# Optimization experiments

Measured on AMD Instinct MI355X. Metric: run time of the kernel, lower is better.

## Reference

```python
import jax, jax.numpy as jnp
import numpy as np

B, N, P, H, E, M, O, T = 4, 128, 512, 64, 32, 64, 64, 64

def _normalize(v, axis=-1, eps=1e-12):
    n = jnp.sqrt(jnp.sum(v * v, axis=axis, keepdims=True))
    return v / jnp.maximum(n, eps)

def _quat_mul(a, b):
    aw, ax, ay, az = a[..., 0], a[..., 1], a[..., 2], a[..., 3]
    bw, bx, by, bz = b[..., 0], b[..., 1], b[..., 2], b[..., 3]
    return jnp.stack([
        aw*bw - ax*bx - ay*by - az*bz,
        aw*bx + ax*bw + ay*bz - az*by,
        aw*by - ax*bz + ay*bw + az*bx,
        aw*bz + ax*by - ay*bx + az*bw], axis=-1)

def _quat_conj(q):
    return q * jnp.array([1.0, -1.0, -1.0, -1.0], dtype=q.dtype)

def _quat_rotate(q, v):
    # rotate vectors v [...,3] by unit quaternions q [...,4] in (w,x,y,z)
    qv = q[..., 1:]
    w = q[..., :1]
    t = 2.0 * jnp.cross(qv, v)
    return v + w * t + jnp.cross(qv, t)

def _mlp(x, W1, b1, W2, b2):
    return jax.nn.relu(x @ W1 + b1) @ W2 + b2

def setup_inputs():
    key = jax.random.key(0)
    ks = jax.random.split(key, 20)
    def w(k, i, o):
        return (jax.random.normal(k, (i, o), jnp.float32) / np.sqrt(i)).astype(jnp.float32)
    inp = dict(
        q=_normalize(jax.random.normal(ks[0], (B, N, 4), jnp.float32)),
        x=jax.random.normal(ks[1], (B, N, 3), jnp.float32),
        torsions=jax.random.normal(ks[2], (B, N, 7, 2), jnp.float32),
        h=jax.random.normal(ks[3], (B, N, H), jnp.float32),
        e=jax.random.normal(ks[4], (B, N, N, E), jnp.float32),
        node_mask=jnp.ones((B, N), bool),
        pocket_q=_normalize(jax.random.normal(ks[5], (B, P, 4), jnp.float32)),
        pocket_x=jax.random.normal(ks[6], (B, P, 3), jnp.float32),
        pocket_e=jax.random.normal(ks[7], (B, N, P, E), jnp.float32),
        pocket_h=jax.random.normal(ks[8], (B, P, H), jnp.float32),
        pocket_mask=jnp.ones((B, P), bool),
        Wm1=w(ks[9], 2 * H + E + 9, T), bm1=jnp.zeros((T,), jnp.float32),
        Wm2=w(ks[10], T, M), bm2=jnp.zeros((M,), jnp.float32),
        Wf1=w(ks[11], H + M, T), bf1=jnp.zeros((T,), jnp.float32),
        Wf2=w(ks[12], T, O), bf2=jnp.zeros((O,), jnp.float32),
        Wx1=w(ks[13], M, T), bx1=jnp.zeros((T,), jnp.float32),
        Wx2=w(ks[14], T, 3), bx2=jnp.zeros((3,), jnp.float32),
        Wq1=w(ks[15], M, T), bq1=jnp.zeros((T,), jnp.float32),
        Wq2=w(ks[16], T, 4), bq2=jnp.zeros((4,), jnp.float32),
        Wt1=w(ks[17], M, T), bt1=jnp.zeros((T,), jnp.float32),
        Wt2=w(ks[18], T, 14), bt2=jnp.zeros((14,), jnp.float32),
    )
    return inp

def _forward(q, x, torsions, h, e, pocket_q, pocket_x, pocket_e, pocket_h,
             node_mask, pocket_mask,
             Wm1, bm1, Wm2, bm2, Wf1, bf1, Wf2, bf2,
             Wx1, bx1, Wx2, bx2, Wq1, bq1, Wq2, bq2, Wt1, bt1, Wt2, bt2):
    b, n, hd = h.shape
    p = pocket_h.shape[-2]
    eye = jnp.eye(n, dtype=bool)
    pep_mm = node_mask[:, :, None] & node_mask[:, None, :] & (~eye)[None]
    poc_mm = node_mask[:, :, None] & pocket_mask[:, None, :]
    msg_mask = jnp.concatenate([pep_mm, poc_mm], axis=-1).astype(h.dtype)  # [B,N,N+P]
    n_neigh = (node_mask.sum(-1) + pocket_mask.sum(-1) - 1).astype(h.dtype)

    all_x = jnp.concatenate([x, pocket_x], axis=-2)   # [B,N+P,3]
    all_q = jnp.concatenate([q, pocket_q], axis=-2)   # [B,N+P,4]

    diff = x[:, :, None, :] - all_x[:, None, :, :]    # [B,N,N+P,3]
    d2 = jnp.sum(diff * diff, axis=-1)                # [B,N,N+P] == cat(peptide_d2, pocket_d2)
    qdot = jnp.abs(jnp.sum(q[:, :, None, :] * all_q[:, None, :, :], axis=-1))
    conj_j = _quat_conj(all_q)[:, None, :, :]         # inverse of frame j rotation
    local_x = _quat_rotate(conj_j, diff)              # R_j^T (x_i - x_j): global_to_local.apply
    local_q = _quat_mul(conj_j, q[:, :, None, :])     # q_j^{-1} * q_i

    hi = jnp.broadcast_to(h[:, :, None, :], (b, n, n + p, hd))
    hj = jnp.broadcast_to(jnp.concatenate([h, pocket_h], axis=-2)[:, None, :, :], (b, n, n + p, hd))
    e_all = jnp.concatenate([e, pocket_e], axis=-2)

    feat = jnp.concatenate([hi, hj, e_all, local_x, local_q, d2[..., None], qdot[..., None]], axis=-1)
    m = _mlp(feat, Wm1, bm1, Wm2, bm2) * msg_mask[..., None]
    msum = m.sum(axis=-2)                             # [B,N,M]

    o = _mlp(jnp.concatenate([h, msum], axis=-1), Wf1, bf1, Wf2, bf2)
    upd_torsions = _normalize(_mlp(msum, Wt1, bt1, Wt2, bt2).reshape(torsions.shape))

    dx = _mlp(m, Wx1, bx1, Wx2, bx2) * msg_mask[..., None]
    dq = _mlp(msum, Wq1, bq1, Wq2, bq2)
    ident = jnp.array([1.0, 0.0, 0.0, 0.0], dtype=dq.dtype)
    dq = jnp.where(node_mask[..., None], dq, ident)
    dq = _normalize(dq)
    upd_q = _quat_mul(q, dq)
    upd_q = jnp.where(node_mask[..., None], upd_q, ident)
    upd_q = _normalize(upd_q)                         # Rigid(Rotation(..., normalize_quats=True))

    rot_j = _normalize(all_q)[:, None, :, :]          # local->global rotation, normalize_quats=True
    upd_x = x + _quat_rotate(rot_j, dx).sum(axis=-2) / n_neigh[:, None, None]
    return upd_q, upd_x, upd_torsions, o

def reference(q, x, torsions, h, e, node_mask, pocket_q, pocket_x, pocket_e, pocket_h, pocket_mask,
              Wm1, bm1, Wm2, bm2, Wf1, bf1, Wf2, bf2,
              Wx1, bx1, Wx2, bx2, Wq1, bq1, Wq2, bq2, Wt1, bt1, Wt2, bt2):
    return _forward(q, x, torsions, h, e, pocket_q, pocket_x, pocket_e, pocket_h,
                    node_mask, pocket_mask,
                    Wm1, bm1, Wm2, bm2, Wf1, bf1, Wf2, bf2,
                    Wx1, bx1, Wx2, bx2, Wq1, bq1, Wq2, bq2, Wt1, bt1, Wt2, bt2)
```

## Files before the change

### kernel.cpp

```cpp
#include <hip/hip_runtime.h>
#include <stdint.h>

#define NB 4
#define NN 128
#define NP 512
#define NJ 640
#define HD 64
#define ED 32

typedef unsigned short u16;
typedef __attribute__((ext_vector_type(8))) short short8;
typedef __attribute__((ext_vector_type(4))) float f32x4;

#define OFF_Q 0
#define OFF_X 2048
#define OFF_T 3584
#define OFF_O 10752

__device__ __forceinline__ u16 f2bf(float f) {
  union { float f; uint32_t i; } v; v.f = f;
  uint32_t x = v.i;
  return (u16)((x + 0x7FFFu + ((x >> 16) & 1u)) >> 16);
}
__device__ __forceinline__ uint32_t pk2(float a, float b) {
  return (uint32_t)f2bf(a) | ((uint32_t)f2bf(b) << 16);
}

__device__ __forceinline__ int w1row(int k) {
  if (k < 32) return 128 + k;
  if (k < 35) return 160 + (k - 32);
  if (k < 39) return 163 + (k - 35);
  if (k == 39) return 167;
  if (k == 40) return 168;
  if (k < 48) return -1;
  if (k < 112) return 64 + (k - 48);
  return -1;
}

__global__ void __launch_bounds__(256, 1)
egnn_fused(const float* __restrict__ q, const float* __restrict__ x,
           const float* __restrict__ h, const float* __restrict__ e,
           const float* __restrict__ pe, const float* __restrict__ pq,
           const float* __restrict__ px, const float* __restrict__ ph,
           const float* __restrict__ Wm1, const float* __restrict__ bm1,
           const float* __restrict__ Wm2, const float* __restrict__ bm2,
           const float* __restrict__ Wx1, const float* __restrict__ bx1,
           const float* __restrict__ Wx2, const float* __restrict__ bx2,
           const float* __restrict__ Wf1, const float* __restrict__ bf1,
           const float* __restrict__ Wf2, const float* __restrict__ bf2_,
           const float* __restrict__ Wq1, const float* __restrict__ bq1,
           const float* __restrict__ Wq2, const float* __restrict__ bq2,
           const float* __restrict__ Wt1, const float* __restrict__ bt1,
           const float* __restrict__ Wt2, const float* __restrict__ bt2,
           float* __restrict__ out)
{
  __shared__ u16 sW1B[64 * 136];
  __shared__ u16 sW2B[64 * 72];
  __shared__ u16 sWx1B[64 * 72];
  __shared__ u16 sWx2B[16 * 72];
  __shared__ u16 sF[4][16 * 136];
  __shared__ u16 sT[4][16 * 72];
  __shared__ float sDxT[4][16][4];
  __shared__ float sMsum[4][64];
  __shared__ float sDx[4][3];
  __shared__ float sHi64[64];
  __shared__ float sHiP[64];
  __shared__ float sPh3[4][64];

  const int b = blockIdx.x >> 7;
  const int i = blockIdx.x & 127;
  const int tid = threadIdx.x;
  const int wid = tid >> 6;
  const int lane = tid & 63;
  const int nl = lane & 15;
  const int quad = lane >> 4;
  const size_t node = (size_t)(b * NN + i);

  u16* sFw = sF[wid];
  u16* sTw = sT[wid];

  for (int idx = tid; idx < 64 * 128; idx += 256) {
    int n = idx >> 7, k = idx & 127;
    int row = w1row(k);
    sW1B[n * 136 + k] = (row < 0) ? (u16)0 : f2bf(Wm1[(size_t)row * 64 + n]);
  }
  for (int idx = tid; idx < 64 * 64; idx += 256) {
    int n = idx >> 6, k = idx & 63;
    sW2B[n * 72 + k]  = f2bf(Wm2[(size_t)k * 64 + n]);
    sWx1B[n * 72 + k] = f2bf(Wx1[(size_t)k * 64 + n]);
  }
  for (int idx = tid; idx < 16 * 64; idx += 256) {
    int n = idx >> 6, k = idx & 63;
    sWx2B[n * 72 + k] = (n < 3) ? f2bf(Wx2[(size_t)k * 3 + n]) : (u16)0;
  }
  for (int idx = lane; idx < 16 * 136 / 2; idx += 64) ((uint32_t*)sFw)[idx] = 0;

  if (tid < 64) sHi64[tid] = h[node * HD + tid];
  if (tid >= 64 && tid < 128) {
    int col = tid - 64;
    float acc = bm1[col];
#pragma unroll 8
    for (int k = 0; k < HD; ++k) acc += h[node * HD + k] * Wm1[k * 64 + col];
    sHiP[col] = acc;
  }

  const float* qr0 = q + node * 4;
  const float qi0 = qr0[0], qi1 = qr0[1], qi2 = qr0[2], qi3 = qr0[3];
  const float* xr0 = x + node * 3;
  const float xi0 = xr0[0], xi1 = xr0[1], xi2 = xr0[2];

  __syncthreads();

  short8 W2f[4][2], Wx1f[4][2], Wx2f[2];
#pragma unroll
  for (int nt = 0; nt < 4; ++nt)
#pragma unroll
    for (int ks = 0; ks < 2; ++ks) {
      W2f[nt][ks]  = *(const short8*)&sW2B[(nt * 16 + nl) * 72 + ks * 32 + quad * 8];
      Wx1f[nt][ks] = *(const short8*)&sWx1B[(nt * 16 + nl) * 72 + ks * 32 + quad * 8];
    }
#pragma unroll
  for (int ks = 0; ks < 2; ++ks)
    Wx2f[ks] = *(const short8*)&sWx2B[nl * 72 + ks * 32 + quad * 8];

  float HiF[4], bm2F[4], bx1F[4];
#pragma unroll
  for (int nt = 0; nt < 4; ++nt) {
    HiF[nt] = sHiP[nt * 16 + nl];
    bm2F[nt] = bm2[nt * 16 + nl];
    bx1F[nt] = bx1[nt * 16 + nl];
  }
  const float bx2F = (nl < 3) ? bx2[nl] : 0.f;

  f32x4 msum[4];
#pragma unroll
  for (int nt = 0; nt < 4; ++nt) msum[nt] = (f32x4){0.f, 0.f, 0.f, 0.f};
  float dxs0 = 0.f, dxs1 = 0.f, dxs2 = 0.f;
  float nqw = 0.f, nqx = 0.f, nqy = 0.f, nqz = 0.f;

  for (int tile = wid; tile < 40; tile += 4) {
    const int jb = tile * 16;
    {
      int er = lane >> 2, c = lane & 3;
      int jr = jb + er;
      const float* ebase = (jr < NN)
          ? e + ((node * NN) + jr) * ED + c * 8
          : pe + ((node * NP) + (jr - NN)) * ED + c * 8;
      float4 e0 = *(const float4*)ebase;
      float4 e1 = *(const float4*)(ebase + 4);
      uint4 pw;
      pw.x = pk2(e0.x, e0.y); pw.y = pk2(e0.z, e0.w);
      pw.z = pk2(e1.x, e1.y); pw.w = pk2(e1.z, e1.w);
      *(uint4*)&sFw[er * 136 + c * 8] = pw;

      const float* hb = (jr < NN) ? h + ((size_t)(b * NN + jr)) * HD + c * 16
                                  : ph + ((size_t)(b * NP + (jr - NN))) * HD + c * 16;
      float4 h0 = *(const float4*)hb, h1 = *(const float4*)(hb + 4);
      float4 h2 = *(const float4*)(hb + 8), h3 = *(const float4*)(hb + 12);
      uint4 pa, pb;
      pa.x = pk2(h0.x, h0.y); pa.y = pk2(h0.z, h0.w);
      pa.z = pk2(h1.x, h1.y); pa.w = pk2(h1.z, h1.w);
      pb.x = pk2(h2.x, h2.y); pb.y = pk2(h2.z, h2.w);
      pb.z = pk2(h3.x, h3.y); pb.w = pk2(h3.z, h3.w);
      *(uint4*)&sFw[er * 136 + 48 + c * 16] = pa;
      *(uint4*)&sFw[er * 136 + 56 + c * 16] = pb;

      if (lane < 16) {
        int j = jb + lane;
        const float* qr = (j < NN) ? q + ((size_t)(b * NN + j)) * 4
                                   : pq + ((size_t)(b * NP + (j - NN))) * 4;
        float4 qj = *(const float4*)qr;
        const float* xr = (j < NN) ? x + ((size_t)(b * NN + j)) * 3
                                   : px + ((size_t)(b * NP + (j - NN))) * 3;
        float xj0 = xr[0], xj1 = xr[1], xj2 = xr[2];
        float d0 = xi0 - xj0, d1 = xi1 - xj1, d2v = xi2 - xj2;
        float d2 = d0 * d0 + d1 * d1 + d2v * d2v;
        float qdot = fabsf(qi0 * qj.x + qi1 * qj.y + qi2 * qj.z + qi3 * qj.w);
        float ajw = qj.x, ajx = -qj.y, ajy = -qj.z, ajz = -qj.w;
        float t0 = 2.f * (ajy * d2v - ajz * d1);
        float t1 = 2.f * (ajz * d0 - ajx * d2v);
        float t2 = 2.f * (ajx * d1 - ajy * d0);
        float lx0 = d0 + ajw * t0 + (ajy * t2 - ajz * t1);
        float lx1 = d1 + ajw * t1 + (ajz * t0 - ajx * t2);
        float lx2 = d2v + ajw * t2 + (ajx * t1 - ajy * t0);
        float lqw = ajw * qi0 - ajx * qi1 - ajy * qi2 - ajz * qi3;
        float lqx = ajw * qi1 + ajx * qi0 + ajy * qi3 - ajz * qi2;
        float lqy = ajw * qi2 - ajx * qi3 + ajy * qi0 + ajz * qi1;
        float lqz = ajw * qi3 + ajx * qi2 - ajy * qi1 + ajz * qi0;
        float nn2 = qj.x * qj.x + qj.y * qj.y + qj.z * qj.z + qj.w * qj.w;
        float rn = 1.f / fmaxf(sqrtf(nn2), 1e-12f);
        nqw = qj.x * rn; nqx = qj.y * rn; nqy = qj.z * rn; nqz = qj.w * rn;
        uint4 g0, g1;
        g0.x = pk2(lx0, lx1); g0.y = pk2(lx2, lqw);
        g0.z = pk2(lqx, lqy); g0.w = pk2(lqz, d2);
        g1.x = pk2(qdot, 0.f); g1.y = 0; g1.z = 0; g1.w = 0;
        *(uint4*)&sFw[lane * 136 + 32] = g0;
        *(uint4*)&sFw[lane * 136 + 40] = g1;
      }
    }

    f32x4 acc[4];
#pragma unroll
    for (int nt = 0; nt < 4; ++nt)
      acc[nt] = (f32x4){HiF[nt], HiF[nt], HiF[nt], HiF[nt]};
#pragma unroll
    for (int ks = 0; ks < 4; ++ks) {
      short8 af = *(const short8*)&sFw[nl * 136 + ks * 32 + quad * 8];
#pragma unroll
      for (int nt = 0; nt < 4; ++nt) {
        short8 bfr = *(const short8*)&sW1B[(nt * 16 + nl) * 136 + ks * 32 + quad * 8];
        acc[nt] = __builtin_amdgcn_mfma_f32_16x16x32_bf16(af, bfr, acc[nt], 0, 0, 0);
      }
    }
#pragma unroll
    for (int nt = 0; nt < 4; ++nt)
#pragma unroll
      for (int r = 0; r < 4; ++r)
        sTw[(quad * 4 + r) * 72 + nt * 16 + nl] = f2bf(fmaxf(acc[nt][r], 0.f));

#pragma unroll
    for (int nt = 0; nt < 4; ++nt)
      acc[nt] = (f32x4){bm2F[nt], bm2F[nt], bm2F[nt], bm2F[nt]};
#pragma unroll
    for (int ks = 0; ks < 2; ++ks) {
      short8 af = *(const short8*)&sTw[nl * 72 + ks * 32 + quad * 8];
#pragma unroll
      for (int nt = 0; nt < 4; ++nt)
        acc[nt] = __builtin_amdgcn_mfma_f32_16x16x32_bf16(af, W2f[nt][ks], acc[nt], 0, 0, 0);
    }
#pragma unroll
    for (int nt = 0; nt < 4; ++nt)
#pragma unroll
      for (int r = 0; r < 4; ++r) {
        int row = quad * 4 + r;
        float v = acc[nt][r];
        if (jb + row == i) v = 0.f;
        msum[nt][r] += v;
        sTw[row * 72 + nt * 16 + nl] = f2bf(v);
      }

#pragma unroll
    for (int nt = 0; nt < 4; ++nt)
      acc[nt] = (f32x4){bx1F[nt], bx1F[nt], bx1F[nt], bx1F[nt]};
#pragma unroll
    for (int ks = 0; ks < 2; ++ks) {
      short8 af = *(const short8*)&sTw[nl * 72 + ks * 32 + quad * 8];
#pragma unroll
      for (int nt = 0; nt < 4; ++nt)
        acc[nt] = __builtin_amdgcn_mfma_f32_16x16x32_bf16(af, Wx1f[nt][ks], acc[nt], 0, 0, 0);
    }
#pragma unroll
    for (int nt = 0; nt < 4; ++nt)
#pragma unroll
      for (int r = 0; r < 4; ++r)
        sTw[(quad * 4 + r) * 72 + nt * 16 + nl] = f2bf(fmaxf(acc[nt][r], 0.f));

    f32x4 dacc = (f32x4){bx2F, bx2F, bx2F, bx2F};
#pragma unroll
    for (int ks = 0; ks < 2; ++ks) {
      short8 af = *(const short8*)&sTw[nl * 72 + ks * 32 + quad * 8];
      dacc = __builtin_amdgcn_mfma_f32_16x16x32_bf16(af, Wx2f[ks], dacc, 0, 0, 0);
    }
    if (nl < 3) {
#pragma unroll
      for (int r = 0; r < 4; ++r) sDxT[wid][quad * 4 + r][nl] = dacc[r];
    }
    if (lane < 16) {
      int j = jb + lane;
      if (j != i) {
        float dxc0 = sDxT[wid][lane][0];
        float dxc1 = sDxT[wid][lane][1];
        float dxc2 = sDxT[wid][lane][2];
        float rt0 = 2.f * (nqy * dxc2 - nqz * dxc1);
        float rt1 = 2.f * (nqz * dxc0 - nqx * dxc2);
        float rt2 = 2.f * (nqx * dxc1 - nqy * dxc0);
        dxs0 += dxc0 + nqw * rt0 + (nqy * rt2 - nqz * rt1);
        dxs1 += dxc1 + nqw * rt1 + (nqz * rt0 - nqx * rt2);
        dxs2 += dxc2 + nqw * rt2 + (nqx * rt1 - nqy * rt0);
      }
    }
  }

#pragma unroll
  for (int nt = 0; nt < 4; ++nt) {
    float s = msum[nt][0] + msum[nt][1] + msum[nt][2] + msum[nt][3];
    s += __shfl_xor(s, 16);
    s += __shfl_xor(s, 32);
    if (lane < 16) sMsum[wid][nt * 16 + lane] = s;
  }
  {
    float a = dxs0, bb = dxs1, cc = dxs2;
#pragma unroll
    for (int off = 1; off < 16; off <<= 1) {
      a += __shfl_xor(a, off);
      bb += __shfl_xor(bb, off);
      cc += __shfl_xor(cc, off);
    }
    if (lane == 0) { sDx[wid][0] = a; sDx[wid][1] = bb; sDx[wid][2] = cc; }
  }
  __syncthreads();

  if (wid == 0) {
    float ms = sMsum[0][lane] + sMsum[1][lane] + sMsum[2][lane] + sMsum[3][lane];
    sPh3[0][lane] = ms;
    float f1a = bf1[lane], f1b = 0.f;
#pragma unroll 8
    for (int k = 0; k < 64; ++k) {
      f1a += sHi64[k] * Wf1[k * 64 + lane];
      f1b += sPh3[0][k] * Wf1[(64 + k) * 64 + lane];
    }
    float f1 = fmaxf(f1a + f1b, 0.f);
    sPh3[0][lane] = f1;
    float oacc = bf2_[lane];
#pragma unroll 8
    for (int k = 0; k < 64; ++k) oacc += sPh3[0][k] * Wf2[k * 64 + lane];
    out[OFF_O + node * 64 + lane] = oacc;
  } else if (wid == 1) {
    float ms = sMsum[0][lane] + sMsum[1][lane] + sMsum[2][lane] + sMsum[3][lane];
    sPh3[1][lane] = ms;
    float a = bq1[lane];
#pragma unroll 8
    for (int k = 0; k < 64; ++k) a += sPh3[1][k] * Wq1[k * 64 + lane];
    a = fmaxf(a, 0.f);
    float p0 = a * Wq2[lane * 4 + 0];
    float p1 = a * Wq2[lane * 4 + 1];
    float p2 = a * Wq2[lane * 4 + 2];
    float p3 = a * Wq2[lane * 4 + 3];
#pragma unroll
    for (int off = 32; off >= 1; off >>= 1) {
      p0 += __shfl_xor(p0, off);
      p1 += __shfl_xor(p1, off);
      p2 += __shfl_xor(p2, off);
      p3 += __shfl_xor(p3, off);
    }
    float dq0 = p0 + bq2[0], dq1 = p1 + bq2[1];
    float dq2 = p2 + bq2[2], dq3 = p3 + bq2[3];
    float n = fmaxf(sqrtf(dq0 * dq0 + dq1 * dq1 + dq2 * dq2 + dq3 * dq3), 1e-12f);
    dq0 /= n; dq1 /= n; dq2 /= n; dq3 /= n;
    float uw = qi0 * dq0 - qi1 * dq1 - qi2 * dq2 - qi3 * dq3;
    float ux = qi0 * dq1 + qi1 * dq0 + qi2 * dq3 - qi3 * dq2;
    float uy = qi0 * dq2 - qi1 * dq3 + qi2 * dq0 + qi3 * dq1;
    float uz = qi0 * dq3 + qi1 * dq2 - qi2 * dq1 + qi3 * dq0;
    float n2 = fmaxf(sqrtf(uw * uw + ux * ux + uy * uy + uz * uz), 1e-12f);
    if (lane == 0) {
      float* po = out + OFF_Q + node * 4;
      po[0] = uw / n2; po[1] = ux / n2; po[2] = uy / n2; po[3] = uz / n2;
    }
  } else if (wid == 2) {
    float ms = sMsum[0][lane] + sMsum[1][lane] + sMsum[2][lane] + sMsum[3][lane];
    sPh3[2][lane] = ms;
    float a = bt1[lane];
#pragma unroll 8
    for (int k = 0; k < 64; ++k) a += sPh3[2][k] * Wt1[k * 64 + lane];
    a = fmaxf(a, 0.f);
    sPh3[2][lane] = a;
    if (lane < 14) {
      float v = bt2[lane];
#pragma unroll 8
      for (int k = 0; k < 64; ++k) v += sPh3[2][k] * Wt2[k * 14 + lane];
      float pv = __shfl_xor(v, 1);
      float nrm = fmaxf(sqrtf(v * v + pv * pv), 1e-12f);
      out[OFF_T + node * 14 + lane] = v / nrm;
    }
  } else {
    if (lane < 3) {
      float xs = sDx[0][lane] + sDx[1][lane] + sDx[2][lane] + sDx[3][lane];
      float xiv = (lane == 0) ? xi0 : (lane == 1) ? xi1 : xi2;
      out[OFF_X + node * 3 + lane] = xiv + xs / 639.0f;
    }
  }
}

extern "C" void kernel_launch(void* const* d_in, const int* in_sizes, int n_in,
                              void* d_out, int out_size, void* d_ws, size_t ws_size,
                              hipStream_t stream) {
  const float* q   = (const float*)d_in[0];
  const float* x   = (const float*)d_in[1];
  const float* h   = (const float*)d_in[3];
  const float* e   = (const float*)d_in[4];
  const float* pq  = (const float*)d_in[6];
  const float* px  = (const float*)d_in[7];
  const float* pe  = (const float*)d_in[8];
  const float* ph  = (const float*)d_in[9];
  const float* Wm1 = (const float*)d_in[11];
  const float* bm1 = (const float*)d_in[12];
  const float* Wm2 = (const float*)d_in[13];
  const float* bm2 = (const float*)d_in[14];
  const float* Wf1 = (const float*)d_in[15];
  const float* bf1 = (const float*)d_in[16];
  const float* Wf2 = (const float*)d_in[17];
  const float* bf2_ = (const float*)d_in[18];
  const float* Wx1 = (const float*)d_in[19];
  const float* bx1 = (const float*)d_in[20];
  const float* Wx2 = (const float*)d_in[21];
  const float* bx2 = (const float*)d_in[22];
  const float* Wq1 = (const float*)d_in[23];
  const float* bq1 = (const float*)d_in[24];
  const float* Wq2 = (const float*)d_in[25];
  const float* bq2 = (const float*)d_in[26];
  const float* Wt1 = (const float*)d_in[27];
  const float* bt1 = (const float*)d_in[28];
  const float* Wt2 = (const float*)d_in[29];
  const float* bt2 = (const float*)d_in[30];

  egnn_fused<<<NB * NN, 256, 0, stream>>>(
      q, x, h, e, pe, pq, px, ph,
      Wm1, bm1, Wm2, bm2, Wx1, bx1, Wx2, bx2,
      Wf1, bf1, Wf2, bf2_, Wq1, bq1, Wq2, bq2,
      Wt1, bt1, Wt2, bt2, (float*)d_out);
}
```

Before: 186.9 us.

## Use 512-thread blocks with eight waves sharing an aliased LDS union

```diff
diff --git a/kernel.cpp b/kernel.cpp
--- a/kernel.cpp
+++ b/kernel.cpp
@@ -37,7 +37,7 @@
   return -1;
 }
 
-__global__ void __launch_bounds__(256, 1)
+__global__ void __launch_bounds__(512, 4)
 egnn_fused(const float* __restrict__ q, const float* __restrict__ x,
            const float* __restrict__ h, const float* __restrict__ e,
            const float* __restrict__ pe, const float* __restrict__ pq,
@@ -55,14 +55,10 @@
            float* __restrict__ out)
 {
   __shared__ u16 sW1B[64 * 136];
-  __shared__ u16 sW2B[64 * 72];
-  __shared__ u16 sWx1B[64 * 72];
-  __shared__ u16 sWx2B[16 * 72];
-  __shared__ u16 sF[4][16 * 136];
-  __shared__ u16 sT[4][16 * 72];
-  __shared__ float sDxT[4][16][4];
-  __shared__ float sMsum[4][64];
-  __shared__ float sDx[4][3];
+  __shared__ __align__(16) u16 sUnion[26624];
+  __shared__ float sDxT[8][16][4];
+  __shared__ float sMsum[8][64];
+  __shared__ float sDx[8][4];
   __shared__ float sHi64[64];
   __shared__ float sHiP[64];
   __shared__ float sPh3[4][64];
@@ -76,24 +72,26 @@
   const int quad = lane >> 4;
   const size_t node = (size_t)(b * NN + i);
 
-  u16* sFw = sF[wid];
-  u16* sTw = sT[wid];
-
-  for (int idx = tid; idx < 64 * 128; idx += 256) {
+  u16* sW2B  = sUnion;
+  u16* sWx1B = sUnion + 4608;
+  u16* sWx2B = sUnion + 9216;
+  u16* sFw = sUnion + wid * 2176;
+  u16* sTw = sUnion + 17408 + wid * 1152;
+
+  for (int idx = tid; idx < 64 * 128; idx += 512) {
     int n = idx >> 7, k = idx & 127;
     int row = w1row(k);
     sW1B[n * 136 + k] = (row < 0) ? (u16)0 : f2bf(Wm1[(size_t)row * 64 + n]);
   }
-  for (int idx = tid; idx < 64 * 64; idx += 256) {
+  for (int idx = tid; idx < 64 * 64; idx += 512) {
     int n = idx >> 6, k = idx & 63;
     sW2B[n * 72 + k]  = f2bf(Wm2[(size_t)k * 64 + n]);
     sWx1B[n * 72 + k] = f2bf(Wx1[(size_t)k * 64 + n]);
   }
-  for (int idx = tid; idx < 16 * 64; idx += 256) {
+  for (int idx = tid; idx < 16 * 64; idx += 512) {
     int n = idx >> 6, k = idx & 63;
     sWx2B[n * 72 + k] = (n < 3) ? f2bf(Wx2[(size_t)k * 3 + n]) : (u16)0;
   }
-  for (int idx = lane; idx < 16 * 136 / 2; idx += 64) ((uint32_t*)sFw)[idx] = 0;
 
   if (tid < 64) sHi64[tid] = h[node * HD + tid];
   if (tid >= 64 && tid < 128) {
@@ -132,13 +130,17 @@
   }
   const float bx2F = (nl < 3) ? bx2[nl] : 0.f;
 
+  __syncthreads();
+
+  for (int idx = lane; idx < 16 * 136 / 2; idx += 64) ((uint32_t*)sFw)[idx] = 0;
+
   f32x4 msum[4];
 #pragma unroll
   for (int nt = 0; nt < 4; ++nt) msum[nt] = (f32x4){0.f, 0.f, 0.f, 0.f};
   float dxs0 = 0.f, dxs1 = 0.f, dxs2 = 0.f;
   float nqw = 0.f, nqx = 0.f, nqy = 0.f, nqz = 0.f;
 
-  for (int tile = wid; tile < 40; tile += 4) {
+  for (int tile = wid; tile < 40; tile += 8) {
     const int jb = tile * 16;
     {
       int er = lane >> 2, c = lane & 3;
@@ -301,7 +303,9 @@
   __syncthreads();
 
   if (wid == 0) {
-    float ms = sMsum[0][lane] + sMsum[1][lane] + sMsum[2][lane] + sMsum[3][lane];
+    float ms = 0.f;
+#pragma unroll
+    for (int w = 0; w < 8; ++w) ms += sMsum[w][lane];
     sPh3[0][lane] = ms;
     float f1a = bf1[lane], f1b = 0.f;
 #pragma unroll 8
@@ -316,7 +320,9 @@
     for (int k = 0; k < 64; ++k) oacc += sPh3[0][k] * Wf2[k * 64 + lane];
     out[OFF_O + node * 64 + lane] = oacc;
   } else if (wid == 1) {
-    float ms = sMsum[0][lane] + sMsum[1][lane] + sMsum[2][lane] + sMsum[3][lane];
+    float ms = 0.f;
+#pragma unroll
+    for (int w = 0; w < 8; ++w) ms += sMsum[w][lane];
     sPh3[1][lane] = ms;
     float a = bq1[lane];
 #pragma unroll 8
@@ -347,7 +353,9 @@
       po[0] = uw / n2; po[1] = ux / n2; po[2] = uy / n2; po[3] = uz / n2;
     }
   } else if (wid == 2) {
-    float ms = sMsum[0][lane] + sMsum[1][lane] + sMsum[2][lane] + sMsum[3][lane];
+    float ms = 0.f;
+#pragma unroll
+    for (int w = 0; w < 8; ++w) ms += sMsum[w][lane];
     sPh3[2][lane] = ms;
     float a = bt1[lane];
 #pragma unroll 8
@@ -362,9 +370,11 @@
       float nrm = fmaxf(sqrtf(v * v + pv * pv), 1e-12f);
       out[OFF_T + node * 14 + lane] = v / nrm;
     }
-  } else {
+  } else if (wid == 3) {
     if (lane < 3) {
-      float xs = sDx[0][lane] + sDx[1][lane] + sDx[2][lane] + sDx[3][lane];
+      float xs = 0.f;
+#pragma unroll
+      for (int w = 0; w < 8; ++w) xs += sDx[w][lane];
       float xiv = (lane == 0) ? xi0 : (lane == 1) ? xi1 : xi2;
       out[OFF_X + node * 3 + lane] = xiv + xs / 639.0f;
     }
@@ -403,7 +413,7 @@
   const float* Wt2 = (const float*)d_in[29];
   const float* bt2 = (const float*)d_in[30];
 
-  egnn_fused<<<NB * NN, 256, 0, stream>>>(
+  egnn_fused<<<NB * NN, 512, 0, stream>>>(
       q, x, h, e, pe, pq, px, ph,
       Wm1, bm1, Wm2, bm2, Wx1, bx1, Wx2, bx2,
       Wf1, bf1, Wf2, bf2_, Wq1, bq1, Wq2, bq2,
```

Result: slower. 252.6 us (+35.1%).
